# Optimization experiments

Measured on AMD Instinct MI355X. Metric: run time of the kernel, lower is better.

Reference implementation:

```python
import jax, jax.numpy as jnp
import numpy as np
from jax.scipy.special import logsumexp


def _lstm(x, mask, Wk, Wr, b, reverse=False):
    # x: [B,T,D], mask: [B,T] bool. Keras LSTM defaults: gate order i,f,g,o,
    # sigmoid recurrent activation, tanh activation. Masked steps carry state.
    if reverse:
        x = x[:, ::-1]
        mask = mask[:, ::-1]
    B, T, _ = x.shape
    H = Wr.shape[0]
    xz = jnp.einsum('btd,dh->bth', x, Wk) + b  # [B,T,4H] input projections, done once

    def step(carry, inp):
        h, c = carry
        z_t, m = inp  # [B,4H], [B]
        z = z_t + h @ Wr
        i, f, g, o = jnp.split(z, 4, axis=-1)
        i = jax.nn.sigmoid(i)
        f = jax.nn.sigmoid(f)
        g = jnp.tanh(g)
        o = jax.nn.sigmoid(o)
        c_new = f * c + i * g
        h_new = o * jnp.tanh(c_new)
        m = m[:, None]
        h = jnp.where(m, h_new, h)
        c = jnp.where(m, c_new, c)
        return (h, c), h

    h0 = jnp.zeros((B, H), x.dtype)
    (_, _), hs = jax.lax.scan(step, (h0, h0), (xz.transpose(1, 0, 2), mask.T))
    hs = hs.transpose(1, 0, 2)  # [B,T,H]
    if reverse:
        hs = hs[:, ::-1]
    return hs


def _crf_log_likelihood(logits, tags, lengths, trans):
    # TFA crf_log_likelihood: sequence_score - log_norm (forward algorithm)
    B, T, C = logits.shape
    t_idx = jnp.arange(T)
    mask = t_idx[None, :] < lengths[:, None]  # [B,T]
    # unary score: sum_t logits[b,t,tags[b,t]] over valid t
    unary = jnp.take_along_axis(logits, tags[..., None], axis=2)[..., 0]
    unary = jnp.sum(jnp.where(mask, unary, 0.0), axis=1)
    # binary score: sum_t trans[tags[t], tags[t+1]] for t < len-1
    binary = trans[tags[:, :-1], tags[:, 1:]]  # [B,T-1]
    mask2 = t_idx[None, : T - 1] < (lengths - 1)[:, None]
    binary = jnp.sum(jnp.where(mask2, binary, 0.0), axis=1)
    # log normalizer via forward algorithm scan
    alpha0 = logits[:, 0]  # [B,C]

    def step(alpha, inp):
        logit_t, m = inp  # [B,C], [B]
        new = logsumexp(alpha[:, :, None] + trans[None], axis=1) + logit_t
        alpha = jnp.where(m[:, None], new, alpha)
        return alpha, None

    alpha, _ = jax.lax.scan(step, alpha0,
                            (logits[:, 1:].transpose(1, 0, 2), mask[:, 1:].T))
    log_norm = logsumexp(alpha, axis=1)
    return unary + binary - log_norm


def setup_inputs() -> dict:
    key = jax.random.key(0)
    ks = jax.random.split(key, 12)
    V, D, H, C, B, T = 30000, 300, 256, 9, 64, 512
    lengths = jax.random.randint(ks[0], (B,), T // 4, T + 1).astype(jnp.int32)
    valid = jnp.arange(T)[None, :] < lengths[:, None]
    inputs = (jax.random.randint(ks[1], (B, T), 1, V) * valid).astype(jnp.int32)
    targets = (jax.random.randint(ks[2], (B, T), 0, C) * valid).astype(jnp.int32)
    s = 0.05
    return {
        'inputs': inputs,
        'inputs_length': lengths,
        'targets': targets,
        'embedding': jax.random.normal(ks[3], (V, D), jnp.float32) * s,
        'Wk_f': jax.random.normal(ks[4], (D, 4 * H), jnp.float32) * s,
        'Wr_f': jax.random.normal(ks[5], (H, 4 * H), jnp.float32) * s,
        'b_f': jnp.zeros((4 * H,), jnp.float32),
        'Wk_b': jax.random.normal(ks[6], (D, 4 * H), jnp.float32) * s,
        'Wr_b': jax.random.normal(ks[7], (H, 4 * H), jnp.float32) * s,
        'b_b': jnp.zeros((4 * H,), jnp.float32),
        'dense_W': jax.random.normal(ks[8], (2 * H, C), jnp.float32) * s,
        'dense_b': jnp.zeros((C,), jnp.float32),
        'trans': jax.random.uniform(ks[9], (C, C), jnp.float32),
    }


def reference(inputs, inputs_length, targets, embedding, Wk_f, Wr_f, b_f,
              Wk_b, Wr_b, b_b, dense_W, dense_b, trans):
    T = inputs.shape[1]
    mask = jnp.arange(T)[None, :] < inputs_length[:, None]  # [B,T]
    emb = embedding[inputs]  # [B,T,D] (dropout is identity in inference)
    h_f = _lstm(emb, mask, Wk_f, Wr_f, b_f, reverse=False)
    h_b = _lstm(emb, mask, Wk_b, Wr_b, b_b, reverse=True)
    h = jnp.concatenate([h_f, h_b], axis=-1)  # [B,T,2H]
    logits = h @ dense_W + dense_b  # [B,T,C]
    log_likelihood = _crf_log_likelihood(logits, targets, inputs_length, trans)
    return logits, log_likelihood, trans
```

## Files before the change

kernel.cpp:

```cpp
#include <hip/hip_runtime.h>
#include <cstdint>
#include <cstddef>

typedef unsigned int  u32;
typedef unsigned short u16;
typedef _Float16 f16;
typedef _Float16 f16x2 __attribute__((ext_vector_type(2)));
typedef _Float16 half8 __attribute__((ext_vector_type(8)));
typedef float    f32x4v __attribute__((ext_vector_type(4)));
typedef int      i32x4 __attribute__((ext_vector_type(4)));

#define BATCH 64
#define TSEQ  512
#define DEMB  300
#define KPAD  320
#define HDIM  256
#define G4    1024
#define NCLS  9

__device__ __forceinline__ u32 packf16(float a, float b) {
  f16x2 v; v.x = (f16)a; v.y = (f16)b;
  return __builtin_bit_cast(u32, v);
}
__device__ __forceinline__ float f16f(u16 x) {
  return (float)__builtin_bit_cast(f16, x);
}
__device__ __forceinline__ float sigm_fast(float x) {
  return __builtin_amdgcn_rcpf(1.f + __expf(-x));
}
__device__ __forceinline__ float tanh_fast(float x) {
  float ax = __builtin_fabsf(x);
  float e = __expf(-2.f * ax);
  float t = (1.f - e) * __builtin_amdgcn_rcpf(1.f + e);
  return copysignf(t, x);
}

__global__ __launch_bounds__(256) void embcvt_k(const float* __restrict__ emb,
                                                u16* __restrict__ out) {
  const int v  = blockIdx.x * 16 + (threadIdx.x >> 4);
  const int kc = threadIdx.x & 15;
  u32* __restrict__ dst = (u32*)(out + (size_t)v * KPAD + kc * 20);
  if (kc < 15) {
    const float* __restrict__ src = emb + (size_t)v * DEMB + kc * 20;
    float tmp[20];
#pragma unroll
    for (int j = 0; j < 20; ++j) tmp[j] = src[j];
#pragma unroll
    for (int j = 0; j < 10; ++j) dst[j] = packf16(tmp[2 * j], tmp[2 * j + 1]);
  } else {
#pragma unroll
    for (int j = 0; j < 10; ++j) dst[j] = 0u;
  }
}

__global__ __launch_bounds__(256) void wkt_k(const float* __restrict__ Wk_f,
                                             const float* __restrict__ Wk_b,
                                             u16* __restrict__ wkt) {
  const int dir = blockIdx.y;
  const float* __restrict__ Wk = dir ? Wk_b : Wk_f;
  const int col = blockIdx.x * 16 + (threadIdx.x >> 4);
  const int kc  = threadIdx.x & 15;
  u32* __restrict__ dst = (u32*)(wkt + ((size_t)dir * G4 + col) * KPAD + kc * 20);
  if (kc < 15) {
    float tmp[20];
#pragma unroll
    for (int j = 0; j < 20; ++j) tmp[j] = Wk[(size_t)(kc * 20 + j) * G4 + col];
#pragma unroll
    for (int j = 0; j < 10; ++j) dst[j] = packf16(tmp[2 * j], tmp[2 * j + 1]);
  } else {
#pragma unroll
    for (int j = 0; j < 10; ++j) dst[j] = 0u;
  }
}

__global__ __launch_bounds__(256) void wr8_k(const float* __restrict__ Wr_f,
                                             const float* __restrict__ Wr_b,
                                             signed char* __restrict__ wr8) {
  const int dir = blockIdx.y;
  const float* __restrict__ Wr = dir ? Wr_b : Wr_f;
  const int col = blockIdx.x * 16 + (threadIdx.x >> 4);
  const int k0  = (threadIdx.x & 15) * 16;
  float tmp[16];
#pragma unroll
  for (int j = 0; j < 16; ++j) tmp[j] = Wr[(size_t)(k0 + j) * G4 + col];
  u32 pw[4];
#pragma unroll
  for (int jj = 0; jj < 4; ++jj) {
    u32 p = 0;
#pragma unroll
    for (int b = 0; b < 4; ++b) {
      int q = (int)__builtin_rintf(tmp[4 * jj + b] * 512.f);
      q = q > 127 ? 127 : (q < -127 ? -127 : q);
      p |= ((u32)(q & 255)) << (8 * b);
    }
    pw[jj] = p;
  }
  *(uint4*)(wr8 + ((size_t)dir * G4 + col) * HDIM + k0) =
      make_uint4(pw[0], pw[1], pw[2], pw[3]);
}

__global__ __launch_bounds__(256) void xz_gemm_k(
    const int* __restrict__ inputs, const u16* __restrict__ wkt,
    const u16* __restrict__ embf16, const float* __restrict__ b_f,
    const float* __restrict__ b_b, u16* __restrict__ xz)
{
  __shared__ __align__(16) u16 As[128 * 40];
  __shared__ __align__(16) u16 Bs[128 * 40];
  const int tid  = threadIdx.x;
  const int wv   = tid >> 6, lane = tid & 63;
  const int quad = lane >> 4, fl = lane & 15;
  const int cbi  = blockIdx.x;
  const int dir  = cbi >> 3;
  const int cb1  = (cbi & 7) * 128;
  const int rb   = blockIdx.y * 128;
  const float* __restrict__ bias = dir ? b_b : b_f;

  const int sm = tid >> 1, sh = (tid & 1) * 16;
  const int vrow = inputs[rb + sm];
  const u16* __restrict__ asrc = wkt + ((size_t)(dir * G4) + cb1 + sm) * KPAD + sh;
  const u16* __restrict__ bsrc = embf16 + (size_t)vrow * KPAD + sh;

  f32x4v acc[2][8];
#pragma unroll
  for (int bt = 0; bt < 2; ++bt)
#pragma unroll
    for (int i = 0; i < 8; ++i) acc[bt][i] = (f32x4v){0.f, 0.f, 0.f, 0.f};

  for (int kt = 0; kt < 10; ++kt) {
    const int k0 = kt * 32;
    uint4 a0v = *(const uint4*)(asrc + k0);
    uint4 a1v = *(const uint4*)(asrc + k0 + 8);
    uint4 b0v = *(const uint4*)(bsrc + k0);
    uint4 b1v = *(const uint4*)(bsrc + k0 + 8);
    *(uint4*)&As[sm * 40 + sh]     = a0v;
    *(uint4*)&As[sm * 40 + sh + 8] = a1v;
    *(uint4*)&Bs[sm * 40 + sh]     = b0v;
    *(uint4*)&Bs[sm * 40 + sh + 8] = b1v;
    __syncthreads();
    half8 bf[2];
#pragma unroll
    for (int bt = 0; bt < 2; ++bt)
      bf[bt] = *(const half8*)&Bs[(wv * 32 + bt * 16 + fl) * 40 + quad * 8];
#pragma unroll
    for (int i = 0; i < 8; ++i) {
      half8 af = *(const half8*)&As[(i * 16 + fl) * 40 + quad * 8];
      acc[0][i] = __builtin_amdgcn_mfma_f32_16x16x32_f16(af, bf[0], acc[0][i], 0, 0, 0);
      acc[1][i] = __builtin_amdgcn_mfma_f32_16x16x32_f16(af, bf[1], acc[1][i], 0, 0, 0);
    }
    __syncthreads();
  }
#pragma unroll
  for (int bt = 0; bt < 2; ++bt) {
    const int row = rb + wv * 32 + bt * 16 + fl;
    u16* __restrict__ orow = xz + ((size_t)(dir * BATCH * TSEQ) + row) * G4;
#pragma unroll
    for (int i = 0; i < 8; ++i) {
      const int mb = cb1 + i * 16 + quad * 4;
      const float4 bb = *(const float4*)&bias[mb];
      f32x4v v = acc[bt][i];
      uint2 pk;
      pk.x = packf16(v[0] + bb.x, v[1] + bb.y);
      pk.y = packf16(v[2] + bb.z, v[3] + bb.w);
      *(uint2*)&orow[mb] = pk;
    }
  }
}

#define MFI(a, b, c) __builtin_amdgcn_mfma_i32_16x16x64_i8(a, b, c, 0, 0, 0)
#define LD8(g, ct, kc) (*(const i32x4*)(wr8w + (size_t)((g) * 256 + 32 * w + (ct) * 16 + l15) * HDIM + (kc) * 64 + q16))
#define DECL8(g, ct) \
  i32x4 W##g##ct##_0 = LD8(g, ct, 0), W##g##ct##_1 = LD8(g, ct, 1), \
        W##g##ct##_2 = LD8(g, ct, 2), W##g##ct##_3 = LD8(g, ct, 3); \
  asm volatile("" : "+a"(W##g##ct##_0), "+a"(W##g##ct##_1), \
                    "+a"(W##g##ct##_2), "+a"(W##g##ct##_3));
#define TILE(g, ct) \
  i32x4 ac##g##ct = (i32x4){0, 0, 0, 0}; \
  ac##g##ct = MFI(af0, W##g##ct##_0, ac##g##ct); \
  ac##g##ct = MFI(af1, W##g##ct##_1, ac##g##ct); \
  ac##g##ct = MFI(af2, W##g##ct##_2, ac##g##ct); \
  ac##g##ct = MFI(af3, W##g##ct##_3, ac##g##ct);

__global__ __launch_bounds__(512, 2) void lstm_k(
    const u16* __restrict__ xz, const signed char* __restrict__ wr8,
    const int* __restrict__ lengths, u16* __restrict__ hcat)
{
  const int chain = blockIdx.x;
  const int dir   = chain >> 6;
  const int batch = chain & 63;
  const int tid  = threadIdx.x;
  const int w    = tid >> 6;
  const int lane = tid & 63;
  const int quad = lane >> 4, l15 = lane & 15;
  const int q16  = quad * 16;
  const int ctsel = quad & 1;
  const int j    = 32 * w + ctsel * 16 + l15;
  const int wr   = quad < 2;
  const float DEQ = 1.f / (512.f * 127.f);

  __shared__ __align__(16) signed char hpk[2][256];

  const signed char* __restrict__ wr8w = wr8 + (size_t)dir * G4 * HDIM;

  DECL8(0, 0) DECL8(0, 1) DECL8(1, 0) DECL8(1, 1)
  DECL8(2, 0) DECL8(2, 1) DECL8(3, 0) DECL8(3, 1)

  if (tid < 256) hpk[0][tid] = 0;

  float c = 0.f, h = 0.f;
  const int len = lengths[batch];
  const u16* __restrict__ xzb = xz + (size_t)(dir * BATCH + batch) * TSEQ * G4;
  u16* __restrict__ hrow = hcat + (size_t)batch * TSEQ * 512 + dir * 256;
  __syncthreads();

  int tt = dir ? (TSEQ - 1) : 0;
  const int dt = dir ? -1 : 1;
  u16 x0 = xzb[(size_t)tt * G4 + j];
  u16 x1 = xzb[(size_t)tt * G4 + 256 + j];
  u16 x2 = xzb[(size_t)tt * G4 + 512 + j];
  u16 x3 = xzb[(size_t)tt * G4 + 768 + j];

  for (int st = 0; st < TSEQ; ++st) {
    const int ttn = (st == TSEQ - 1) ? tt : tt + dt;
    u16 xn0 = xzb[(size_t)ttn * G4 + j];
    u16 xn1 = xzb[(size_t)ttn * G4 + 256 + j];
    u16 xn2 = xzb[(size_t)ttn * G4 + 512 + j];
    u16 xn3 = xzb[(size_t)ttn * G4 + 768 + j];

    const int par = st & 1;
    const signed char* hb = &hpk[par][0];
    i32x4 af0 = *(const i32x4*)(hb + q16);
    i32x4 af1 = *(const i32x4*)(hb + 64 + q16);
    i32x4 af2 = *(const i32x4*)(hb + 128 + q16);
    i32x4 af3 = *(const i32x4*)(hb + 192 + q16);

    TILE(0, 0) TILE(0, 1)
    TILE(1, 0) TILE(1, 1)
    TILE(2, 0) TILE(2, 1)
    TILE(3, 0) TILE(3, 1)

    int ri = ctsel ? ac01[0] : ac00[0];
    int rf = ctsel ? ac11[0] : ac10[0];
    int rg = ctsel ? ac21[0] : ac20[0];
    int ro = ctsel ? ac31[0] : ac30[0];

    float zi = (float)ri * DEQ + f16f(x0);
    float zf = (float)rf * DEQ + f16f(x1);
    float zg = (float)rg * DEQ + f16f(x2);
    float zo = (float)ro * DEQ + f16f(x3);
    float ig = sigm_fast(zi);
    float fg = sigm_fast(zf);
    float gg = tanh_fast(zg);
    float og = sigm_fast(zo);
    float cn = fg * c + ig * gg;
    float hn = og * tanh_fast(cn);
    if (tt < len) { c = cn; h = hn; }
    if (wr) {
      u32 hb2 = packf16(h, h);
      hrow[(size_t)tt * 512 + j] = (u16)(hb2 & 0xffffu);
      int hq = (int)__builtin_rintf(h * 127.f);
      hpk[par ^ 1][j] = (signed char)hq;
    }
    __syncthreads();
    x0 = xn0; x1 = xn1; x2 = xn2; x3 = xn3; tt = ttn;
  }
}

__global__ __launch_bounds__(256) void dense_k(
    const u16* __restrict__ hcat, const float* __restrict__ W,
    const float* __restrict__ bias, float* __restrict__ out)
{
  const int lane = threadIdx.x & 63;
  const int wv = threadIdx.x >> 6;
  const int rowbase = (blockIdx.x * 4 + wv) * 8;
  for (int rr = 0; rr < 8; ++rr) {
    const int row = rowbase + rr;
    const u16* __restrict__ hr = hcat + (size_t)row * 512;
    float hv[8];
#pragma unroll
    for (int i = 0; i < 8; ++i)
      hv[i] = f16f(hr[i * 64 + lane]);
    float myout = 0.f;
#pragma unroll
    for (int cc = 0; cc < 9; ++cc) {
      float p = 0.f;
#pragma unroll
      for (int i = 0; i < 8; ++i)
        p = fmaf(hv[i], W[(size_t)(i * 64 + lane) * 9 + cc], p);
#pragma unroll
      for (int o = 32; o > 0; o >>= 1) p += __shfl_xor(p, o);
      if (lane == cc) myout = p + bias[cc];
    }
    if (lane < 9) out[(size_t)row * 9 + lane] = myout;
  }
}

__global__ __launch_bounds__(64) void crf_k(
    const float* __restrict__ logits, const int* __restrict__ tags,
    const int* __restrict__ lengths, const float* __restrict__ trans,
    float* __restrict__ out_ll, float* __restrict__ out_trans)
{
  const int b = blockIdx.x;
  const int lane = threadIdx.x;
  const int len = lengths[b];
  const float* __restrict__ lg = logits + (size_t)b * TSEQ * NCLS;
  const int* __restrict__ tg = tags + (size_t)b * TSEQ;

  float ua = 0.f, ba = 0.f;
  for (int t = lane; t < TSEQ; t += 64) {
    int tag = tg[t];
    if (t < len) ua += lg[t * 9 + tag];
    if (t < len - 1) ba += trans[tag * 9 + tg[t + 1]];
  }
  float s = ua + ba;
#pragma unroll
  for (int o = 32; o > 0; o >>= 1) s += __shfl_xor(s, o);

  const int j = (lane < 9) ? lane : 0;
  float trc[9], alpha[9];
#pragma unroll
  for (int i = 0; i < 9; ++i) trc[i] = trans[i * 9 + j];
#pragma unroll
  for (int i = 0; i < 9; ++i) alpha[i] = lg[i];
  for (int t = 1; t < TSEQ; ++t) {
    if (t >= len) break;
    float m = -1e30f;
#pragma unroll
    for (int i = 0; i < 9; ++i) m = fmaxf(m, alpha[i] + trc[i]);
    float ss = 0.f;
#pragma unroll
    for (int i = 0; i < 9; ++i) ss += __expf(alpha[i] + trc[i] - m);
    float nj = __logf(ss) + m + lg[t * 9 + j];
#pragma unroll
    for (int i = 0; i < 9; ++i) alpha[i] = __shfl(nj, i);
  }
  float m2 = -1e30f;
#pragma unroll
  for (int i = 0; i < 9; ++i) m2 = fmaxf(m2, alpha[i]);
  float s2 = 0.f;
#pragma unroll
  for (int i = 0; i < 9; ++i) s2 += __expf(alpha[i] - m2);
  float lse = __logf(s2) + m2;
  if (lane == 0) out_ll[b] = s - lse;
  if (b == 0)
    for (int i = lane; i < 81; i += 64) out_trans[i] = trans[i];
}

extern "C" void kernel_launch(void* const* d_in, const int* in_sizes, int n_in,
                              void* d_out, int out_size, void* d_ws, size_t ws_size,
                              hipStream_t stream)
{
  const int*   inputs  = (const int*)d_in[0];
  const int*   lengths = (const int*)d_in[1];
  const int*   targets = (const int*)d_in[2];
  const float* emb     = (const float*)d_in[3];
  const float* Wk_f    = (const float*)d_in[4];
  const float* Wr_f    = (const float*)d_in[5];
  const float* b_f     = (const float*)d_in[6];
  const float* Wk_b    = (const float*)d_in[7];
  const float* Wr_b    = (const float*)d_in[8];
  const float* b_b     = (const float*)d_in[9];
  const float* dense_W = (const float*)d_in[10];
  const float* dense_b = (const float*)d_in[11];
  const float* trans   = (const float*)d_in[12];

  char* ws = (char*)d_ws;
  u16*         wkt    = (u16*)ws;
  signed char* wr8    = (signed char*)(ws + 1310720ull);
  u16*         embf16 = (u16*)(ws + 1835008ull);
  u16*         xz     = (u16*)(ws + 1835008ull + 19200000ull);
  u16*         hcat   = (u16*)(ws + 1835008ull + 19200000ull + 134217728ull);

  float* out_logits = (float*)d_out;
  float* out_ll     = out_logits + (size_t)BATCH * TSEQ * NCLS;
  float* out_trans  = out_ll + BATCH;

  hipLaunchKernelGGL(embcvt_k, dim3(1875), dim3(256), 0, stream, emb, embf16);
  hipLaunchKernelGGL(wkt_k, dim3(64, 2), dim3(256), 0, stream, Wk_f, Wk_b, wkt);
  hipLaunchKernelGGL(wr8_k, dim3(64, 2), dim3(256), 0, stream, Wr_f, Wr_b, wr8);
  hipLaunchKernelGGL(xz_gemm_k, dim3(16, 256), dim3(256), 0, stream,
                     inputs, wkt, embf16, b_f, b_b, xz);
  hipLaunchKernelGGL(lstm_k, dim3(128), dim3(512), 0, stream,
                     xz, wr8, lengths, hcat);
  hipLaunchKernelGGL(dense_k, dim3(1024), dim3(256), 0, stream,
                     hcat, dense_W, dense_b, out_logits);
  hipLaunchKernelGGL(crf_k, dim3(64), dim3(64), 0, stream,
                     out_logits, targets, lengths, trans, out_ll, out_trans);
}
```

Before: 722.0 us.

## Split LSTM recurrent work across 16 waves, one 16-column tile each

The recurrent LSTM kernel now launches 1024 threads per chain instead of 512. Each of the 16 waves owns a single 16-column hidden tile across all four gates, rather than two tiles per wave across 8 waves. This halves the serial MFMA chain per wave and interleaves the four gate accumulators so independent MFMAs can overlap. It also raises wave priority around the MFMA block. In exchange, only one quad per wave writes results, and the per-step barrier now synchronises twice as many waves.

After: 799.8 us. +10.8%, slower.

```diff
diff --git a/kernel.cpp b/kernel.cpp
--- a/kernel.cpp
+++ b/kernel.cpp
@@ -167,20 +167,14 @@
 }
 
 #define MFI(a, b, c) __builtin_amdgcn_mfma_i32_16x16x64_i8(a, b, c, 0, 0, 0)
-#define LD8(g, ct, kc) (*(const i32x4*)(wr8w + (size_t)((g) * 256 + 32 * w + (ct) * 16 + l15) * HDIM + (kc) * 64 + q16))
-#define DECL8(g, ct) \
-  i32x4 W##g##ct##_0 = LD8(g, ct, 0), W##g##ct##_1 = LD8(g, ct, 1), \
-        W##g##ct##_2 = LD8(g, ct, 2), W##g##ct##_3 = LD8(g, ct, 3); \
-  asm volatile("" : "+a"(W##g##ct##_0), "+a"(W##g##ct##_1), \
-                    "+a"(W##g##ct##_2), "+a"(W##g##ct##_3));
-#define TILE(g, ct) \
-  i32x4 ac##g##ct = (i32x4){0, 0, 0, 0}; \
-  ac##g##ct = MFI(af0, W##g##ct##_0, ac##g##ct); \
-  ac##g##ct = MFI(af1, W##g##ct##_1, ac##g##ct); \
-  ac##g##ct = MFI(af2, W##g##ct##_2, ac##g##ct); \
-  ac##g##ct = MFI(af3, W##g##ct##_3, ac##g##ct);
-
-__global__ __launch_bounds__(512, 2) void lstm_k(
+#define LDW(g, kc) (*(const i32x4*)(wr8w + (size_t)((g) * 256 + jj) * HDIM + (kc) * 64 + q16))
+#define DECLW(g) \
+  i32x4 W##g##_0 = LDW(g, 0), W##g##_1 = LDW(g, 1), \
+        W##g##_2 = LDW(g, 2), W##g##_3 = LDW(g, 3); \
+  asm volatile("" : "+a"(W##g##_0), "+a"(W##g##_1), \
+                    "+a"(W##g##_2), "+a"(W##g##_3));
+
+__global__ __launch_bounds__(1024, 4) void lstm_k(
     const u16* __restrict__ xz, const signed char* __restrict__ wr8,
     const int* __restrict__ lengths, u16* __restrict__ hcat)
 {
@@ -192,17 +186,15 @@
   const int lane = tid & 63;
   const int quad = lane >> 4, l15 = lane & 15;
   const int q16  = quad * 16;
-  const int ctsel = quad & 1;
-  const int j    = 32 * w + ctsel * 16 + l15;
-  const int wr   = quad < 2;
+  const int jj   = (w << 4) + l15;
+  const int wr   = (quad == 0);
   const float DEQ = 1.f / (512.f * 127.f);
 
   __shared__ __align__(16) signed char hpk[2][256];
 
   const signed char* __restrict__ wr8w = wr8 + (size_t)dir * G4 * HDIM;
 
-  DECL8(0, 0) DECL8(0, 1) DECL8(1, 0) DECL8(1, 1)
-  DECL8(2, 0) DECL8(2, 1) DECL8(3, 0) DECL8(3, 1)
+  DECLW(0) DECLW(1) DECLW(2) DECLW(3)
 
   if (tid < 256) hpk[0][tid] = 0;
 
@@ -214,17 +206,17 @@
 
   int tt = dir ? (TSEQ - 1) : 0;
   const int dt = dir ? -1 : 1;
-  u16 x0 = xzb[(size_t)tt * G4 + j];
-  u16 x1 = xzb[(size_t)tt * G4 + 256 + j];
-  u16 x2 = xzb[(size_t)tt * G4 + 512 + j];
-  u16 x3 = xzb[(size_t)tt * G4 + 768 + j];
+  u16 x0 = xzb[(size_t)tt * G4 + jj];
+  u16 x1 = xzb[(size_t)tt * G4 + 256 + jj];
+  u16 x2 = xzb[(size_t)tt * G4 + 512 + jj];
+  u16 x3 = xzb[(size_t)tt * G4 + 768 + jj];
 
   for (int st = 0; st < TSEQ; ++st) {
     const int ttn = (st == TSEQ - 1) ? tt : tt + dt;
-    u16 xn0 = xzb[(size_t)ttn * G4 + j];
-    u16 xn1 = xzb[(size_t)ttn * G4 + 256 + j];
-    u16 xn2 = xzb[(size_t)ttn * G4 + 512 + j];
-    u16 xn3 = xzb[(size_t)ttn * G4 + 768 + j];
+    u16 xn0 = xzb[(size_t)ttn * G4 + jj];
+    u16 xn1 = xzb[(size_t)ttn * G4 + 256 + jj];
+    u16 xn2 = xzb[(size_t)ttn * G4 + 512 + jj];
+    u16 xn3 = xzb[(size_t)ttn * G4 + 768 + jj];
 
     const int par = st & 1;
     const signed char* hb = &hpk[par][0];
@@ -233,20 +225,25 @@
     i32x4 af2 = *(const i32x4*)(hb + 128 + q16);
     i32x4 af3 = *(const i32x4*)(hb + 192 + q16);
 
-    TILE(0, 0) TILE(0, 1)
-    TILE(1, 0) TILE(1, 1)
-    TILE(2, 0) TILE(2, 1)
-    TILE(3, 0) TILE(3, 1)
-
-    int ri = ctsel ? ac01[0] : ac00[0];
-    int rf = ctsel ? ac11[0] : ac10[0];
-    int rg = ctsel ? ac21[0] : ac20[0];
-    int ro = ctsel ? ac31[0] : ac30[0];
-
-    float zi = (float)ri * DEQ + f16f(x0);
-    float zf = (float)rf * DEQ + f16f(x1);
-    float zg = (float)rg * DEQ + f16f(x2);
-    float zo = (float)ro * DEQ + f16f(x3);
+    i32x4 a0 = (i32x4){0, 0, 0, 0};
+    i32x4 a1 = (i32x4){0, 0, 0, 0};
+    i32x4 a2 = (i32x4){0, 0, 0, 0};
+    i32x4 a3 = (i32x4){0, 0, 0, 0};
+    __builtin_amdgcn_s_setprio(1);
+    a0 = MFI(af0, W0_0, a0); a1 = MFI(af0, W1_0, a1);
+    a2 = MFI(af0, W2_0, a2); a3 = MFI(af0, W3_0, a3);
+    a0 = MFI(af1, W0_1, a0); a1 = MFI(af1, W1_1, a1);
+    a2 = MFI(af1, W2_1, a2); a3 = MFI(af1, W3_1, a3);
+    a0 = MFI(af2, W0_2, a0); a1 = MFI(af2, W1_2, a1);
+    a2 = MFI(af2, W2_2, a2); a3 = MFI(af2, W3_2, a3);
+    a0 = MFI(af3, W0_3, a0); a1 = MFI(af3, W1_3, a1);
+    a2 = MFI(af3, W2_3, a2); a3 = MFI(af3, W3_3, a3);
+    __builtin_amdgcn_s_setprio(0);
+
+    float zi = (float)a0[0] * DEQ + f16f(x0);
+    float zf = (float)a1[0] * DEQ + f16f(x1);
+    float zg = (float)a2[0] * DEQ + f16f(x2);
+    float zo = (float)a3[0] * DEQ + f16f(x3);
     float ig = sigm_fast(zi);
     float fg = sigm_fast(zf);
     float gg = tanh_fast(zg);
@@ -256,9 +253,9 @@
     if (tt < len) { c = cn; h = hn; }
     if (wr) {
       u32 hb2 = packf16(h, h);
-      hrow[(size_t)tt * 512 + j] = (u16)(hb2 & 0xffffu);
+      hrow[(size_t)tt * 512 + jj] = (u16)(hb2 & 0xffffu);
       int hq = (int)__builtin_rintf(h * 127.f);
-      hpk[par ^ 1][j] = (signed char)hq;
+      hpk[par ^ 1][jj] = (signed char)hq;
     }
     __syncthreads();
     x0 = xn0; x1 = xn1; x2 = xn2; x3 = xn3; tt = ttn;
@@ -379,7 +376,7 @@
   hipLaunchKernelGGL(wr8_k, dim3(64, 2), dim3(256), 0, stream, Wr_f, Wr_b, wr8);
   hipLaunchKernelGGL(xz_gemm_k, dim3(16, 256), dim3(256), 0, stream,
                      inputs, wkt, embf16, b_f, b_b, xz);
-  hipLaunchKernelGGL(lstm_k, dim3(128), dim3(512), 0, stream,
+  hipLaunchKernelGGL(lstm_k, dim3(128), dim3(1024), 0, stream,
                      xz, wr8, lengths, hcat);
   hipLaunchKernelGGL(dense_k, dim3(1024), dim3(256), 0, stream,
                      hcat, dense_W, dense_b, out_logits);
```

## Replace MFMA recurrent matvec with per-thread int8 dot4 over register-resident weights

Applied to the files above, without the earlier changes.

The LSTM recurrent step no longer uses int8 MFMA tiles, where most of each 16x16 output tile was wasted on a single batch row. Each thread now keeps two full int8 weight rows (gate columns) in VGPRs and computes its two gate pre-activations with v_dot4_i32_i8 against the shared int8 hidden vector. Thread pairs split the four gates (i,g on even lanes, f,o on odd lanes) and exchange the i*g product with a shuffle. This removes redundant matrix-core work and the lane-select overhead, at the cost of 128 VGPRs of weights per thread and 64 serial-ish dot4s per step.

Result: slower. 788.0 us (+9.2%).

```diff
diff --git a/kernel.cpp b/kernel.cpp
--- a/kernel.cpp
+++ b/kernel.cpp
@@ -33,6 +33,15 @@
   float e = __expf(-2.f * ax);
   float t = (1.f - e) * __builtin_amdgcn_rcpf(1.f + e);
   return copysignf(t, x);
+}
+__device__ __forceinline__ int sdot4(int a, int b, int c) {
+#if __has_builtin(__builtin_amdgcn_sdot4)
+  return __builtin_amdgcn_sdot4(a, b, c, false);
+#else
+  int r;
+  asm volatile("v_dot4_i32_i8 %0, %1, %2, %3" : "=v"(r) : "v"(a), "v"(b), "v"(c));
+  return r;
+#endif
 }
 
 __global__ __launch_bounds__(256) void embcvt_k(const float* __restrict__ emb,
@@ -166,20 +175,6 @@
   }
 }
 
-#define MFI(a, b, c) __builtin_amdgcn_mfma_i32_16x16x64_i8(a, b, c, 0, 0, 0)
-#define LD8(g, ct, kc) (*(const i32x4*)(wr8w + (size_t)((g) * 256 + 32 * w + (ct) * 16 + l15) * HDIM + (kc) * 64 + q16))
-#define DECL8(g, ct) \
-  i32x4 W##g##ct##_0 = LD8(g, ct, 0), W##g##ct##_1 = LD8(g, ct, 1), \
-        W##g##ct##_2 = LD8(g, ct, 2), W##g##ct##_3 = LD8(g, ct, 3); \
-  asm volatile("" : "+a"(W##g##ct##_0), "+a"(W##g##ct##_1), \
-                    "+a"(W##g##ct##_2), "+a"(W##g##ct##_3));
-#define TILE(g, ct) \
-  i32x4 ac##g##ct = (i32x4){0, 0, 0, 0}; \
-  ac##g##ct = MFI(af0, W##g##ct##_0, ac##g##ct); \
-  ac##g##ct = MFI(af1, W##g##ct##_1, ac##g##ct); \
-  ac##g##ct = MFI(af2, W##g##ct##_2, ac##g##ct); \
-  ac##g##ct = MFI(af3, W##g##ct##_3, ac##g##ct);
-
 __global__ __launch_bounds__(512, 2) void lstm_k(
     const u16* __restrict__ xz, const signed char* __restrict__ wr8,
     const int* __restrict__ lengths, u16* __restrict__ hcat)
@@ -187,22 +182,24 @@
   const int chain = blockIdx.x;
   const int dir   = chain >> 6;
   const int batch = chain & 63;
-  const int tid  = threadIdx.x;
-  const int w    = tid >> 6;
-  const int lane = tid & 63;
-  const int quad = lane >> 4, l15 = lane & 15;
-  const int q16  = quad * 16;
-  const int ctsel = quad & 1;
-  const int j    = 32 * w + ctsel * 16 + l15;
-  const int wr   = quad < 2;
+  const int tid   = threadIdx.x;
+  const int odd   = tid & 1;
+  const int hidx  = tid >> 1;
+  const int c0    = odd * 256 + hidx;
+  const int c1    = c0 + 512;
   const float DEQ = 1.f / (512.f * 127.f);
 
   __shared__ __align__(16) signed char hpk[2][256];
 
   const signed char* __restrict__ wr8w = wr8 + (size_t)dir * G4 * HDIM;
 
-  DECL8(0, 0) DECL8(0, 1) DECL8(1, 0) DECL8(1, 1)
-  DECL8(2, 0) DECL8(2, 1) DECL8(3, 0) DECL8(3, 1)
+  i32x4 w0[16], w1[16];
+#pragma unroll
+  for (int j = 0; j < 16; ++j) {
+    w0[j] = *(const i32x4*)(wr8w + (size_t)c0 * HDIM + j * 16);
+    w1[j] = *(const i32x4*)(wr8w + (size_t)c1 * HDIM + j * 16);
+    asm volatile("" : "+v"(w0[j]), "+v"(w1[j]));
+  }
 
   if (tid < 256) hpk[0][tid] = 0;
 
@@ -214,54 +211,62 @@
 
   int tt = dir ? (TSEQ - 1) : 0;
   const int dt = dir ? -1 : 1;
-  u16 x0 = xzb[(size_t)tt * G4 + j];
-  u16 x1 = xzb[(size_t)tt * G4 + 256 + j];
-  u16 x2 = xzb[(size_t)tt * G4 + 512 + j];
-  u16 x3 = xzb[(size_t)tt * G4 + 768 + j];
+  u16 x0 = xzb[(size_t)tt * G4 + c0];
+  u16 x1 = xzb[(size_t)tt * G4 + c1];
 
   for (int st = 0; st < TSEQ; ++st) {
     const int ttn = (st == TSEQ - 1) ? tt : tt + dt;
-    u16 xn0 = xzb[(size_t)ttn * G4 + j];
-    u16 xn1 = xzb[(size_t)ttn * G4 + 256 + j];
-    u16 xn2 = xzb[(size_t)ttn * G4 + 512 + j];
-    u16 xn3 = xzb[(size_t)ttn * G4 + 768 + j];
+    u16 xn0 = xzb[(size_t)ttn * G4 + c0];
+    u16 xn1 = xzb[(size_t)ttn * G4 + c1];
 
     const int par = st & 1;
     const signed char* hb = &hpk[par][0];
-    i32x4 af0 = *(const i32x4*)(hb + q16);
-    i32x4 af1 = *(const i32x4*)(hb + 64 + q16);
-    i32x4 af2 = *(const i32x4*)(hb + 128 + q16);
-    i32x4 af3 = *(const i32x4*)(hb + 192 + q16);
-
-    TILE(0, 0) TILE(0, 1)
-    TILE(1, 0) TILE(1, 1)
-    TILE(2, 0) TILE(2, 1)
-    TILE(3, 0) TILE(3, 1)
-
-    int ri = ctsel ? ac01[0] : ac00[0];
-    int rf = ctsel ? ac11[0] : ac10[0];
-    int rg = ctsel ? ac21[0] : ac20[0];
-    int ro = ctsel ? ac31[0] : ac30[0];
-
-    float zi = (float)ri * DEQ + f16f(x0);
-    float zf = (float)rf * DEQ + f16f(x1);
-    float zg = (float)rg * DEQ + f16f(x2);
-    float zo = (float)ro * DEQ + f16f(x3);
-    float ig = sigm_fast(zi);
-    float fg = sigm_fast(zf);
-    float gg = tanh_fast(zg);
-    float og = sigm_fast(zo);
-    float cn = fg * c + ig * gg;
-    float hn = og * tanh_fast(cn);
-    if (tt < len) { c = cn; h = hn; }
-    if (wr) {
+
+    int a0p = 0, a0q = 0, a1p = 0, a1q = 0;
+#pragma unroll
+    for (int ch = 0; ch < 4; ++ch) {
+      i32x4 hv[4];
+#pragma unroll
+      for (int q = 0; q < 4; ++q)
+        hv[q] = *(const i32x4*)(hb + ch * 64 + q * 16);
+#pragma unroll
+      for (int q = 0; q < 4; ++q) {
+#pragma unroll
+        for (int e = 0; e < 4; ++e) {
+          if (((q * 4 + e) & 1) == 0) {
+            a0p = sdot4(hv[q][e], w0[ch * 4 + q][e], a0p);
+            a1p = sdot4(hv[q][e], w1[ch * 4 + q][e], a1p);
+          } else {
+            a0q = sdot4(hv[q][e], w0[ch * 4 + q][e], a0q);
+            a1q = sdot4(hv[q][e], w1[ch * 4 + q][e], a1q);
+          }
+        }
+      }
+    }
+    const int s0 = a0p + a0q;
+    const int s1 = a1p + a1q;
+
+    float z0 = (float)s0 * DEQ + f16f(x0);
+    float z1 = (float)s1 * DEQ + f16f(x1);
+    float g0 = sigm_fast(z0);
+    float earg = odd ? -z1 : (-2.f * __builtin_fabsf(z1));
+    float e = __expf(earg);
+    float d = __builtin_amdgcn_rcpf(1.f + e);
+    float g1 = odd ? d : copysignf((1.f - e) * d, z1);
+
+    float P = g0 * g1;
+    float Pin = __shfl_xor(P, 1);
+    if (odd) {
+      float cn = fmaf(g0, c, Pin);
+      float hn = g1 * tanh_fast(cn);
+      if (tt < len) { c = cn; h = hn; }
       u32 hb2 = packf16(h, h);
-      hrow[(size_t)tt * 512 + j] = (u16)(hb2 & 0xffffu);
+      hrow[(size_t)tt * 512 + hidx] = (u16)(hb2 & 0xffffu);
       int hq = (int)__builtin_rintf(h * 127.f);
-      hpk[par ^ 1][j] = (signed char)hq;
+      hpk[par ^ 1][hidx] = (signed char)hq;
     }
     __syncthreads();
-    x0 = xn0; x1 = xn1; x2 = xn2; x3 = xn3; tt = ttn;
+    x0 = xn0; x1 = xn1; tt = ttn;
   }
 }
 
```

## Double-buffer LDS tiles and use 2x2 warp tiling in input-projection GEMM

Applied to the files above, without the earlier changes.

The input projection GEMM now double-buffers its A/B shared-memory tiles. The next k-slice is loaded from global memory while MFMAs run on the current slice, which removes one barrier per iteration. Each wave also computes a 64x64 sub-tile (2x2 wave arrangement) instead of 32 rows by all 128 columns, so LDS fragment reads per MFMA drop. This doubles shared memory use and keeps prefetch registers live across the MFMA block.

After: 708.1 us. Within noise of the previous version (-1.9%).

```diff
diff --git a/kernel.cpp b/kernel.cpp
--- a/kernel.cpp
+++ b/kernel.cpp
@@ -104,11 +104,13 @@
     const u16* __restrict__ embf16, const float* __restrict__ b_f,
     const float* __restrict__ b_b, u16* __restrict__ xz)
 {
-  __shared__ __align__(16) u16 As[128 * 40];
-  __shared__ __align__(16) u16 Bs[128 * 40];
+  __shared__ __align__(16) u16 As[2][128 * 40];
+  __shared__ __align__(16) u16 Bs[2][128 * 40];
   const int tid  = threadIdx.x;
   const int wv   = tid >> 6, lane = tid & 63;
   const int quad = lane >> 4, fl = lane & 15;
+  const int wm   = wv & 1;
+  const int wn   = wv >> 1;
   const int cbi  = blockIdx.x;
   const int dir  = cbi >> 3;
   const int cb1  = (cbi & 7) * 128;
@@ -120,44 +122,67 @@
   const u16* __restrict__ asrc = wkt + ((size_t)(dir * G4) + cb1 + sm) * KPAD + sh;
   const u16* __restrict__ bsrc = embf16 + (size_t)vrow * KPAD + sh;
 
-  f32x4v acc[2][8];
-#pragma unroll
-  for (int bt = 0; bt < 2; ++bt)
-#pragma unroll
-    for (int i = 0; i < 8; ++i) acc[bt][i] = (f32x4v){0.f, 0.f, 0.f, 0.f};
+  f32x4v acc[4][4];
+#pragma unroll
+  for (int i = 0; i < 4; ++i)
+#pragma unroll
+    for (int bt = 0; bt < 4; ++bt) acc[i][bt] = (f32x4v){0.f, 0.f, 0.f, 0.f};
+
+  {
+    uint4 a0v = *(const uint4*)(asrc);
+    uint4 a1v = *(const uint4*)(asrc + 8);
+    uint4 b0v = *(const uint4*)(bsrc);
+    uint4 b1v = *(const uint4*)(bsrc + 8);
+    *(uint4*)&As[0][sm * 40 + sh]     = a0v;
+    *(uint4*)&As[0][sm * 40 + sh + 8] = a1v;
+    *(uint4*)&Bs[0][sm * 40 + sh]     = b0v;
+    *(uint4*)&Bs[0][sm * 40 + sh + 8] = b1v;
+  }
+  __syncthreads();
 
   for (int kt = 0; kt < 10; ++kt) {
-    const int k0 = kt * 32;
-    uint4 a0v = *(const uint4*)(asrc + k0);
-    uint4 a1v = *(const uint4*)(asrc + k0 + 8);
-    uint4 b0v = *(const uint4*)(bsrc + k0);
-    uint4 b1v = *(const uint4*)(bsrc + k0 + 8);
-    *(uint4*)&As[sm * 40 + sh]     = a0v;
-    *(uint4*)&As[sm * 40 + sh + 8] = a1v;
-    *(uint4*)&Bs[sm * 40 + sh]     = b0v;
-    *(uint4*)&Bs[sm * 40 + sh + 8] = b1v;
+    const int cur = kt & 1;
+    uint4 na0, na1, nb0, nb1;
+    if (kt < 9) {
+      const int k0 = (kt + 1) * 32;
+      na0 = *(const uint4*)(asrc + k0);
+      na1 = *(const uint4*)(asrc + k0 + 8);
+      nb0 = *(const uint4*)(bsrc + k0);
+      nb1 = *(const uint4*)(bsrc + k0 + 8);
+    }
+
+    half8 af[4], bf[4];
+#pragma unroll
+    for (int i = 0; i < 4; ++i)
+      af[i] = *(const half8*)&As[cur][(wm * 64 + i * 16 + fl) * 40 + quad * 8];
+#pragma unroll
+    for (int bt = 0; bt < 4; ++bt)
+      bf[bt] = *(const half8*)&Bs[cur][(wn * 64 + bt * 16 + fl) * 40 + quad * 8];
+#pragma unroll
+    for (int i = 0; i < 4; ++i)
+#pragma unroll
+      for (int bt = 0; bt < 4; ++bt)
+        acc[i][bt] = __builtin_amdgcn_mfma_f32_16x16x32_f16(af[i], bf[bt], acc[i][bt], 0, 0, 0);
+
+    if (kt < 9) {
+      const int alt = cur ^ 1;
+      *(uint4*)&As[alt][sm * 40 + sh]     = na0;
+      *(uint4*)&As[alt][sm * 40 + sh + 8] = na1;
+      *(uint4*)&Bs[alt][sm * 40 + sh]     = nb0;
+      *(uint4*)&Bs[alt][sm * 40 + sh + 8] = nb1;
+    }
     __syncthreads();
-    half8 bf[2];
-#pragma unroll
-    for (int bt = 0; bt < 2; ++bt)
-      bf[bt] = *(const half8*)&Bs[(wv * 32 + bt * 16 + fl) * 40 + quad * 8];
-#pragma unroll
-    for (int i = 0; i < 8; ++i) {
-      half8 af = *(const half8*)&As[(i * 16 + fl) * 40 + quad * 8];
-      acc[0][i] = __builtin_amdgcn_mfma_f32_16x16x32_f16(af, bf[0], acc[0][i], 0, 0, 0);
-      acc[1][i] = __builtin_amdgcn_mfma_f32_16x16x32_f16(af, bf[1], acc[1][i], 0, 0, 0);
-    }
-    __syncthreads();
-  }
-#pragma unroll
-  for (int bt = 0; bt < 2; ++bt) {
-    const int row = rb + wv * 32 + bt * 16 + fl;
+  }
+
+#pragma unroll
+  for (int bt = 0; bt < 4; ++bt) {
+    const int row = rb + wn * 64 + bt * 16 + fl;
     u16* __restrict__ orow = xz + ((size_t)(dir * BATCH * TSEQ) + row) * G4;
 #pragma unroll
-    for (int i = 0; i < 8; ++i) {
-      const int mb = cb1 + i * 16 + quad * 4;
+    for (int i = 0; i < 4; ++i) {
+      const int mb = cb1 + wm * 64 + i * 16 + quad * 4;
       const float4 bb = *(const float4*)&bias[mb];
-      f32x4v v = acc[bt][i];
+      f32x4v v = acc[i][bt];
       uint2 pk;
       pk.x = packf16(v[0] + bb.x, v[1] + bb.y);
       pk.y = packf16(v[2] + bb.z, v[3] + bb.w);
```
